# Optimization experiments

Hardware: AMD Instinct MI355X
Metric: run time of the kernel (lower is better)

## Reference

```python
import jax, jax.numpy as jnp
import numpy as np


def setup_inputs() -> dict:
    key = jax.random.key(0)
    k1, k2 = jax.random.split(key)
    N, C, K = 65536, 128, 1024  # N = batch*emb_sample_len flattened latents
    z_e = jax.random.normal(k1, (N, C), dtype=jnp.float32)
    # nn.Embedding codebook; original inits uniform(-1/K, 1/K), randn is fine for a numeric reference
    codebook = jax.random.normal(k2, (K, C), dtype=jnp.float32) * 0.02
    return {"z_e": z_e, "codebook": codebook}


def reference(z_e, codebook):
    """VQ-VAE quantizer core: cdist + argmin nearest-codebook lookup,
    commitment loss (0.75 * q_latent + e_latent), straight-through estimator.
    z_e: [N, C] flattened encoder latents; codebook: [K, C].
    """
    # Squared euclidean distances, expanded form (same argmin as torch.cdist)
    ze_sq = jnp.sum(z_e * z_e, axis=1, keepdims=True)          # [N, 1]
    cb_sq = jnp.sum(codebook * codebook, axis=1)                # [K]
    cross = jnp.einsum('nc,kc->nk', z_e, codebook)              # [N, K]
    dist_sq = ze_sq - 2.0 * cross + cb_sq[None, :]              # [N, K]
    encoding_indices = jnp.argmin(dist_sq, axis=1)              # [N] int

    z_q = codebook[encoding_indices]                            # [N, C] gather

    # commitment loss: 0.75 * mse(stop_grad(z_e), z_q) + mse(z_e, stop_grad(z_q))
    q_latent_loss = jnp.mean((jax.lax.stop_gradient(z_e) - z_q) ** 2)
    e_latent_loss = jnp.mean((z_e - jax.lax.stop_gradient(z_q)) ** 2)
    commitment_loss = 0.75 * q_latent_loss + e_latent_loss

    # straight-through estimator (training path)
    z_q_st = z_e + jax.lax.stop_gradient(z_q - z_e)
    return z_q_st, commitment_loss, encoding_indices
```

## Files before the change

### kernel.cpp

```cpp
#include <hip/hip_runtime.h>

#define N_TOT 65536
#define C_DIM 128
#define K_CB  1024
#define BN 64
#define BT 64
#define NTILE (K_CB / BT)
#define NROW_B 4
#define NBLK_B (N_TOT / NROW_B)

typedef __attribute__((ext_vector_type(8))) short bf16x8;
typedef __attribute__((ext_vector_type(4))) float f32x4;

__device__ __forceinline__ ushort f2bf_rne(float f) {
  unsigned u = __float_as_uint(f);
  return (ushort)((u + 0x7FFFu + ((u >> 16) & 1u)) >> 16);
}

__device__ __forceinline__ unsigned med3u(unsigned a, unsigned b, unsigned c) {
  unsigned d;
  asm("v_med3_u32 %0, %1, %2, %3" : "=v"(d) : "v"(a), "v"(b), "v"(c));
  return d;
}

#define GLDS16(src, dst)                                                       \
  __builtin_amdgcn_global_load_lds(                                            \
      (const __attribute__((address_space(1))) void*)(src),                    \
      (__attribute__((address_space(3))) void*)(dst), 16, 0, 0)

__global__ __launch_bounds__(256) void prep_kernel(
    const float* __restrict__ cb, float* __restrict__ cbsq,
    ushort* __restrict__ cbh) {
  int w = threadIdx.x >> 6, lane = threadIdx.x & 63;
  int r = blockIdx.x * 4 + w;
  float2 v = reinterpret_cast<const float2*>(cb + (size_t)r * C_DIM)[lane];
  ushort2 h;
  h.x = f2bf_rne(v.x); h.y = f2bf_rne(v.y);
  reinterpret_cast<ushort2*>(cbh + (size_t)r * C_DIM)[lane] = h;
  double s = (double)v.x * (double)v.x + (double)v.y * (double)v.y;
#pragma unroll
  for (int off = 32; off >= 1; off >>= 1) s += __shfl_xor(s, off, 64);
  if (lane == 0) cbsq[r] = (float)s;
}

__global__ __launch_bounds__(256, 4) void dist_mfma_kernel(
    const float* __restrict__ ze, const ushort* __restrict__ cbh,
    const float* __restrict__ cbsq, ushort* __restrict__ cand) {
  __shared__ __align__(16) char smem[36864];
  char* const B0 = smem;
  char* const B1 = smem + 16384;
  ushort* zhS = reinterpret_cast<ushort*>(B1);
  unsigned* pool = reinterpret_cast<unsigned*>(smem);
  float* const cbsqS = reinterpret_cast<float*>(smem + 32768);

  const int tid = threadIdx.x;
  const int w = tid >> 6, lane = tid & 63;
  const int mh = w & 1, nh = w >> 1;
  const int c16 = lane & 15, quad = lane >> 4;
  const int rowbase = blockIdx.x * BN;

  int soff[4];
#pragma unroll
  for (int i = 0; i < 4; ++i) {
    int o = w * 4096 + i * 1024 + lane * 16;
    int row = o >> 8, inrow = o & 255;
    soff[i] = row * 256 + (inrow ^ ((row & 7) << 4));
  }
  const int stoff = w * 4096;

#pragma unroll
  for (int i = 0; i < 4; ++i)
    GLDS16((const char*)cbh + soff[i], B0 + stoff + i * 1024);

#pragma unroll
  for (int p = 0; p < 4; ++p) {
    int fid = p * 256 + tid;
    int row = fid >> 4, c8 = fid & 15;
    float4 a = reinterpret_cast<const float4*>(ze)[(size_t)(rowbase + row) * 32 + c8 * 2];
    float4 b = reinterpret_cast<const float4*>(ze)[(size_t)(rowbase + row) * 32 + c8 * 2 + 1];
    ushort h[8] = {f2bf_rne(a.x), f2bf_rne(a.y), f2bf_rne(a.z), f2bf_rne(a.w),
                   f2bf_rne(b.x), f2bf_rne(b.y), f2bf_rne(b.z), f2bf_rne(b.w)};
    *reinterpret_cast<uint4*>(&zhS[row * 128 + ((c8 ^ (row & 7)) * 8)]) =
        *reinterpret_cast<const uint4*>(h);
  }
  reinterpret_cast<float4*>(cbsqS)[tid] = reinterpret_cast<const float4*>(cbsq)[tid];
  __syncthreads();

  const int xk = c16 & 7;
  bf16x8 afrag[2][4];
#pragma unroll
  for (int m2 = 0; m2 < 2; ++m2) {
    int r = (mh * 32 + m2 * 16 + c16) * 128;
#pragma unroll
    for (int ks = 0; ks < 4; ++ks)
      afrag[m2][ks] = *reinterpret_cast<const bf16x8*>(&zhS[r + ((ks * 4 + quad) ^ xk) * 8]);
  }
  __syncthreads();

  unsigned t3[8][3];
#pragma unroll
  for (int s = 0; s < 8; ++s) { t3[s][0] = 0xFFFFFFFFu; t3[s][1] = 0xFFFFFFFFu; t3[s][2] = 0xFFFFFFFFu; }

  const int cbase = nh * 32 + c16;
  const char* cur = B0;
  char* nxt = B1;

  for (int t = 0; t < NTILE; ++t) {
    if (t + 1 < NTILE) {
#pragma unroll
      for (int i = 0; i < 4; ++i)
        GLDS16((const char*)cbh + (size_t)(t + 1) * 16384 + soff[i], nxt + stoff + i * 1024);
    }

    bf16x8 bf[2][4];
#pragma unroll
    for (int n2 = 0; n2 < 2; ++n2) {
      int rb = (nh * 32 + n2 * 16 + c16) * 256;
#pragma unroll
      for (int ks = 0; ks < 4; ++ks)
        bf[n2][ks] = *reinterpret_cast<const bf16x8*>(cur + rb + (((ks * 4 + quad) ^ xk) << 4));
    }

    f32x4 acc[2][2];
#pragma unroll
    for (int m2 = 0; m2 < 2; ++m2)
#pragma unroll
      for (int n2 = 0; n2 < 2; ++n2) acc[m2][n2] = (f32x4){0.f, 0.f, 0.f, 0.f};

#pragma unroll
    for (int ks = 0; ks < 4; ++ks)
#pragma unroll
      for (int m2 = 0; m2 < 2; ++m2)
#pragma unroll
        for (int n2 = 0; n2 < 2; ++n2)
          acc[m2][n2] = __builtin_amdgcn_mfma_f32_16x16x32_bf16(afrag[m2][ks], bf[n2][ks], acc[m2][n2], 0, 0, 0);

#pragma unroll
    for (int n2 = 0; n2 < 2; ++n2) {
      int code = t * BT + cbase + n2 * 16;
      unsigned codeu = (unsigned)code & 1023u;
      float csb = cbsqS[code] + 192.0f;
#pragma unroll
      for (int m2 = 0; m2 < 2; ++m2)
#pragma unroll
        for (int reg = 0; reg < 4; ++reg) {
          float kf = fmaf(-2.f, acc[m2][n2][reg], csb);
          unsigned pk = (__float_as_uint(kf) & 0xFFFFFC00u) | codeu;
          int s = m2 * 4 + reg;
          unsigned n0 = min(t3[s][0], pk);
          unsigned n1 = med3u(t3[s][0], t3[s][1], pk);
          unsigned n2v = med3u(t3[s][1], t3[s][2], pk);
          t3[s][0] = n0; t3[s][1] = n1; t3[s][2] = n2v;
        }
    }

    __syncthreads();
    char* tmp = const_cast<char*>(cur); cur = nxt; nxt = tmp;
  }

#pragma unroll
  for (int s = 0; s < 8; ++s) {
    int row = mh * 32 + (s >> 2) * 16 + quad * 4 + (s & 3);
    int col = (nh * 16 + c16) * 3;
    pool[row * 97 + col] = t3[s][0];
    pool[row * 97 + col + 1] = t3[s][1];
    pool[row * 97 + col + 2] = t3[s][2];
  }
  __syncthreads();
  if (tid < BN) {
    unsigned k[8];
#pragma unroll
    for (int q = 0; q < 8; ++q) k[q] = 0xFFFFFFFFu;
    for (int p = 0; p < 96; ++p) {
      unsigned v = pool[tid * 97 + p];
      if (v < k[7]) {
        k[7] = v;
#pragma unroll
        for (int q = 7; q > 0; --q)
          if (k[q] < k[q - 1]) { unsigned tk = k[q]; k[q] = k[q - 1]; k[q - 1] = tk; }
      }
    }
    uint4 cw;
    cw.x = (k[0] & 1023u) | ((k[1] & 1023u) << 16);
    cw.y = (k[2] & 1023u) | ((k[3] & 1023u) << 16);
    cw.z = (k[4] & 1023u) | ((k[5] & 1023u) << 16);
    cw.w = (k[6] & 1023u) | ((k[7] & 1023u) << 16);
    reinterpret_cast<uint4*>(cand)[rowbase + tid] = cw;
  }
}

__global__ __launch_bounds__(256) void rescore_kernel(
    const float* __restrict__ ze, const float* __restrict__ cb,
    const float* __restrict__ cbsq, const ushort* __restrict__ cand,
    float* __restrict__ zq, float* __restrict__ idx_f,
    double* __restrict__ partial) {
  int w = threadIdx.x >> 6, lane = threadIdx.x & 63;
  int row = blockIdx.x * NROW_B + w;
  int g = lane >> 3, e = lane & 7;
  int myc = cand[(size_t)row * 8 + g];

  float2 z2 = reinterpret_cast<const float2*>(ze)[(size_t)row * 64 + lane];
  double zsum = (double)z2.x * (double)z2.x + (double)z2.y * (double)z2.y;
#pragma unroll
  for (int off = 32; off >= 1; off >>= 1) zsum += __shfl_xor(zsum, off, 64);
  float zs = (float)zsum;

  const float4* zrow4 = reinterpret_cast<const float4*>(ze + (size_t)row * C_DIM);
  const float4* crow4 = reinterpret_cast<const float4*>(cb + (size_t)myc * C_DIM);
  double p = 0.0;
#pragma unroll
  for (int q = 0; q < 4; ++q) {
    float4 zz = zrow4[e * 4 + q];
    float4 cc = crow4[e * 4 + q];
    p += (double)zz.x * (double)cc.x + (double)zz.y * (double)cc.y +
         (double)zz.z * (double)cc.z + (double)zz.w * (double)cc.w;
  }
  p += __shfl_xor(p, 1, 64);
  p += __shfl_xor(p, 2, 64);
  p += __shfl_xor(p, 4, 64);

  float tt = (float)(2.0 * p);
  float u = zs - tt;
  float d = u + cbsq[myc];

  float best = 3.4e38f;
  int bidx = K_CB + 1;
#pragma unroll
  for (int gg = 0; gg < 8; ++gg) {
    float dg = __shfl(d, gg * 8, 64);
    int ig = __shfl(myc, gg * 8, 64);
    if (dg < best || (dg == best && ig < bidx)) { best = dg; bidx = ig; }
  }

  float2 c2 = reinterpret_cast<const float2*>(cb)[(size_t)bidx * 64 + lane];
  reinterpret_cast<float2*>(zq)[(size_t)row * 64 + lane] = c2;

  double dx = (double)z2.x - (double)c2.x;
  double dy = (double)z2.y - (double)c2.y;
  double l = dx * dx + dy * dy;
#pragma unroll
  for (int off = 32; off >= 1; off >>= 1) l += __shfl_xor(l, off, 64);

  __shared__ double sh[NROW_B];
  if (lane == 0) { idx_f[row] = (float)bidx; sh[w] = l; }
  __syncthreads();
  if (threadIdx.x == 0) partial[blockIdx.x] = sh[0] + sh[1] + sh[2] + sh[3];
}

__global__ __launch_bounds__(256) void finalize_kernel(
    const double* __restrict__ partial, float* __restrict__ out_loss) {
  double s = 0.0;
  for (int i = threadIdx.x; i < NBLK_B; i += 256) s += partial[i];
#pragma unroll
  for (int off = 32; off >= 1; off >>= 1) s += __shfl_down(s, off, 64);
  __shared__ double sh[4];
  int wv = threadIdx.x >> 6, lane = threadIdx.x & 63;
  if (lane == 0) sh[wv] = s;
  __syncthreads();
  if (threadIdx.x == 0) {
    double tot = sh[0] + sh[1] + sh[2] + sh[3];
    double mse = tot / (double)((size_t)N_TOT * C_DIM);
    *out_loss = (float)(1.75 * mse);
  }
}

extern "C" void kernel_launch(void* const* d_in, const int* in_sizes, int n_in,
                              void* d_out, int out_size, void* d_ws, size_t ws_size,
                              hipStream_t stream) {
  const float* ze = (const float*)d_in[0];
  const float* cb = (const float*)d_in[1];

  float* out = (float*)d_out;
  float* zq = out;
  float* out_loss = out + (size_t)N_TOT * C_DIM;
  float* idx_f = out_loss + 1;

  float* cbsq = (float*)d_ws;
  ushort* cbh = (ushort*)((char*)d_ws + 8192);
  ushort* cand = (ushort*)((char*)d_ws + 270336);
  double* partial = (double*)((char*)d_ws + 1318912);

  prep_kernel<<<K_CB / 4, 256, 0, stream>>>(cb, cbsq, cbh);
  dist_mfma_kernel<<<N_TOT / BN, 256, 0, stream>>>(ze, cbh, cbsq, cand);
  rescore_kernel<<<NBLK_B, 256, 0, stream>>>(ze, cb, cbsq, cand, zq, idx_f, partial);
  finalize_kernel<<<1, 256, 0, stream>>>(partial, out_loss);
}
```

Before: 165.7 us.

## Software-pipeline distance MFMA with top-k sort and batch two rows per rescore wave

The distance kernel's tile loop is restructured into a two-accumulator software pipeline. The top-3 selection for tile t-1 now runs while the MFMAs for tile t are issued, and the loop is unrolled in pairs over the double buffers. The rescore kernel now has each wave handle two rows, with interleaved reductions and split dot-product accumulators to raise ILP. This halves the rescore block count and the number of partials. In exchange it uses more registers, which may lower occupancy.

Result: faster. 159.2 us (-3.9%).

```diff
diff --git a/kernel.cpp b/kernel.cpp
--- a/kernel.cpp
+++ b/kernel.cpp
@@ -6,8 +6,8 @@
 #define BN 64
 #define BT 64
 #define NTILE (K_CB / BT)
-#define NROW_B 4
-#define NBLK_B (N_TOT / NROW_B)
+#define ROWS_BLK 8
+#define NBLK_R (N_TOT / ROWS_BLK)
 
 typedef __attribute__((ext_vector_type(8))) short bf16x8;
 typedef __attribute__((ext_vector_type(4))) float f32x4;
@@ -102,31 +102,25 @@
   for (int s = 0; s < 8; ++s) { t3[s][0] = 0xFFFFFFFFu; t3[s][1] = 0xFFFFFFFFu; t3[s][2] = 0xFFFFFFFFu; }
 
   const int cbase = nh * 32 + c16;
-  const char* cur = B0;
-  char* nxt = B1;
-
-  for (int t = 0; t < NTILE; ++t) {
-    if (t + 1 < NTILE) {
-#pragma unroll
-      for (int i = 0; i < 4; ++i)
-        GLDS16((const char*)cbh + (size_t)(t + 1) * 16384 + soff[i], nxt + stoff + i * 1024);
-    }
-
+
+  auto STAGE = [&](int t, char* dst) {
+#pragma unroll
+    for (int i = 0; i < 4; ++i)
+      GLDS16((const char*)cbh + (size_t)t * 16384 + soff[i], dst + stoff + i * 1024);
+  };
+  auto READ_MFMA = [&](const char* buf, f32x4 (&acc)[2][2]) {
     bf16x8 bf[2][4];
 #pragma unroll
     for (int n2 = 0; n2 < 2; ++n2) {
       int rb = (nh * 32 + n2 * 16 + c16) * 256;
 #pragma unroll
       for (int ks = 0; ks < 4; ++ks)
-        bf[n2][ks] = *reinterpret_cast<const bf16x8*>(cur + rb + (((ks * 4 + quad) ^ xk) << 4));
-    }
-
-    f32x4 acc[2][2];
+        bf[n2][ks] = *reinterpret_cast<const bf16x8*>(buf + rb + (((ks * 4 + quad) ^ xk) << 4));
+    }
 #pragma unroll
     for (int m2 = 0; m2 < 2; ++m2)
 #pragma unroll
       for (int n2 = 0; n2 < 2; ++n2) acc[m2][n2] = (f32x4){0.f, 0.f, 0.f, 0.f};
-
 #pragma unroll
     for (int ks = 0; ks < 4; ++ks)
 #pragma unroll
@@ -134,7 +128,8 @@
 #pragma unroll
         for (int n2 = 0; n2 < 2; ++n2)
           acc[m2][n2] = __builtin_amdgcn_mfma_f32_16x16x32_bf16(afrag[m2][ks], bf[n2][ks], acc[m2][n2], 0, 0, 0);
-
+  };
+  auto SORT = [&](const f32x4 (&acc)[2][2], int t) {
 #pragma unroll
     for (int n2 = 0; n2 < 2; ++n2) {
       int code = t * BT + cbase + n2 * 16;
@@ -153,10 +148,29 @@
           t3[s][0] = n0; t3[s][1] = n1; t3[s][2] = n2v;
         }
     }
-
+  };
+
+  f32x4 accA[2][2], accB[2][2];
+
+  STAGE(1, B1);
+  READ_MFMA(B0, accA);
+  __syncthreads();
+
+  for (int tp = 0; tp < 7; ++tp) {
+    int t = 2 * tp + 1;
+    STAGE(t + 1, B0);
+    SORT(accA, t - 1);
+    READ_MFMA(B1, accB);
     __syncthreads();
-    char* tmp = const_cast<char*>(cur); cur = nxt; nxt = tmp;
-  }
+    STAGE(t + 2, B1);
+    SORT(accB, t);
+    READ_MFMA(B0, accA);
+    __syncthreads();
+  }
+  SORT(accA, 14);
+  READ_MFMA(B1, accB);
+  SORT(accB, 15);
+  __syncthreads();
 
 #pragma unroll
   for (int s = 0; s < 8; ++s) {
@@ -195,62 +209,105 @@
     float* __restrict__ zq, float* __restrict__ idx_f,
     double* __restrict__ partial) {
   int w = threadIdx.x >> 6, lane = threadIdx.x & 63;
-  int row = blockIdx.x * NROW_B + w;
+  int rbase = blockIdx.x * ROWS_BLK + w * 2;
   int g = lane >> 3, e = lane & 7;
-  int myc = cand[(size_t)row * 8 + g];
-
-  float2 z2 = reinterpret_cast<const float2*>(ze)[(size_t)row * 64 + lane];
-  double zsum = (double)z2.x * (double)z2.x + (double)z2.y * (double)z2.y;
-#pragma unroll
-  for (int off = 32; off >= 1; off >>= 1) zsum += __shfl_xor(zsum, off, 64);
-  float zs = (float)zsum;
-
-  const float4* zrow4 = reinterpret_cast<const float4*>(ze + (size_t)row * C_DIM);
-  const float4* crow4 = reinterpret_cast<const float4*>(cb + (size_t)myc * C_DIM);
-  double p = 0.0;
-#pragma unroll
-  for (int q = 0; q < 4; ++q) {
-    float4 zz = zrow4[e * 4 + q];
-    float4 cc = crow4[e * 4 + q];
-    p += (double)zz.x * (double)cc.x + (double)zz.y * (double)cc.y +
-         (double)zz.z * (double)cc.z + (double)zz.w * (double)cc.w;
-  }
-  p += __shfl_xor(p, 1, 64);
-  p += __shfl_xor(p, 2, 64);
-  p += __shfl_xor(p, 4, 64);
-
-  float tt = (float)(2.0 * p);
-  float u = zs - tt;
-  float d = u + cbsq[myc];
-
-  float best = 3.4e38f;
-  int bidx = K_CB + 1;
+
+  int myc[2];
+  float2 z2[2];
+  double zsum[2];
+#pragma unroll
+  for (int r = 0; r < 2; ++r) {
+    myc[r] = cand[(size_t)(rbase + r) * 8 + g];
+    z2[r] = reinterpret_cast<const float2*>(ze)[(size_t)(rbase + r) * 64 + lane];
+    zsum[r] = (double)z2[r].x * (double)z2[r].x + (double)z2[r].y * (double)z2[r].y;
+  }
+#pragma unroll
+  for (int off = 32; off >= 1; off >>= 1) {
+    zsum[0] += __shfl_xor(zsum[0], off, 64);
+    zsum[1] += __shfl_xor(zsum[1], off, 64);
+  }
+
+  double p[2];
+#pragma unroll
+  for (int r = 0; r < 2; ++r) {
+    const float4* zr = reinterpret_cast<const float4*>(ze + (size_t)(rbase + r) * C_DIM);
+    const float4* cr = reinterpret_cast<const float4*>(cb + (size_t)myc[r] * C_DIM);
+    double p0 = 0.0, p1 = 0.0;
+#pragma unroll
+    for (int q = 0; q < 2; ++q) {
+      float4 zz = zr[e * 4 + q];
+      float4 cc = cr[e * 4 + q];
+      p0 += (double)zz.x * (double)cc.x + (double)zz.y * (double)cc.y +
+            (double)zz.z * (double)cc.z + (double)zz.w * (double)cc.w;
+      float4 zz2 = zr[e * 4 + 2 + q];
+      float4 cc2 = cr[e * 4 + 2 + q];
+      p1 += (double)zz2.x * (double)cc2.x + (double)zz2.y * (double)cc2.y +
+            (double)zz2.z * (double)cc2.z + (double)zz2.w * (double)cc2.w;
+    }
+    p[r] = p0 + p1;
+  }
+#pragma unroll
+  for (int off = 1; off <= 4; off <<= 1) {
+    p[0] += __shfl_xor(p[0], off, 64);
+    p[1] += __shfl_xor(p[1], off, 64);
+  }
+
+  float d[2];
+#pragma unroll
+  for (int r = 0; r < 2; ++r) {
+    float zs = (float)zsum[r];
+    float tt = (float)(2.0 * p[r]);
+    float u = zs - tt;
+    d[r] = u + cbsq[myc[r]];
+  }
+
+  float best[2];
+  int bidx[2];
+#pragma unroll
+  for (int r = 0; r < 2; ++r) { best[r] = 3.4e38f; bidx[r] = K_CB + 1; }
 #pragma unroll
   for (int gg = 0; gg < 8; ++gg) {
-    float dg = __shfl(d, gg * 8, 64);
-    int ig = __shfl(myc, gg * 8, 64);
-    if (dg < best || (dg == best && ig < bidx)) { best = dg; bidx = ig; }
-  }
-
-  float2 c2 = reinterpret_cast<const float2*>(cb)[(size_t)bidx * 64 + lane];
-  reinterpret_cast<float2*>(zq)[(size_t)row * 64 + lane] = c2;
-
-  double dx = (double)z2.x - (double)c2.x;
-  double dy = (double)z2.y - (double)c2.y;
-  double l = dx * dx + dy * dy;
-#pragma unroll
-  for (int off = 32; off >= 1; off >>= 1) l += __shfl_xor(l, off, 64);
-
-  __shared__ double sh[NROW_B];
-  if (lane == 0) { idx_f[row] = (float)bidx; sh[w] = l; }
-  __syncthreads();
-  if (threadIdx.x == 0) partial[blockIdx.x] = sh[0] + sh[1] + sh[2] + sh[3];
+#pragma unroll
+    for (int r = 0; r < 2; ++r) {
+      float dg = __shfl(d[r], gg * 8, 64);
+      int ig = __shfl(myc[r], gg * 8, 64);
+      if (dg < best[r] || (dg == best[r] && ig < bidx[r])) { best[r] = dg; bidx[r] = ig; }
+    }
+  }
+
+  double l[2];
+#pragma unroll
+  for (int r = 0; r < 2; ++r) {
+    float2 c2 = reinterpret_cast<const float2*>(cb)[(size_t)bidx[r] * 64 + lane];
+    reinterpret_cast<float2*>(zq)[(size_t)(rbase + r) * 64 + lane] = c2;
+    double dx = (double)z2[r].x - (double)c2.x;
+    double dy = (double)z2[r].y - (double)c2.y;
+    l[r] = dx * dx + dy * dy;
+  }
+#pragma unroll
+  for (int off = 32; off >= 1; off >>= 1) {
+    l[0] += __shfl_xor(l[0], off, 64);
+    l[1] += __shfl_xor(l[1], off, 64);
+  }
+
+  __shared__ double sh[ROWS_BLK];
+  if (lane == 0) {
+    idx_f[rbase] = (float)bidx[0];
+    idx_f[rbase + 1] = (float)bidx[1];
+    sh[w * 2] = l[0];
+    sh[w * 2 + 1] = l[1];
+  }
+  __syncthreads();
+  if (threadIdx.x == 0) {
+    partial[blockIdx.x] = ((sh[0] + sh[1]) + (sh[2] + sh[3])) +
+                          ((sh[4] + sh[5]) + (sh[6] + sh[7]));
+  }
 }
 
 __global__ __launch_bounds__(256) void finalize_kernel(
     const double* __restrict__ partial, float* __restrict__ out_loss) {
   double s = 0.0;
-  for (int i = threadIdx.x; i < NBLK_B; i += 256) s += partial[i];
+  for (int i = threadIdx.x; i < NBLK_R; i += 256) s += partial[i];
 #pragma unroll
   for (int off = 32; off >= 1; off >>= 1) s += __shfl_down(s, off, 64);
   __shared__ double sh[4];
@@ -282,6 +339,6 @@
 
   prep_kernel<<<K_CB / 4, 256, 0, stream>>>(cb, cbsq, cbh);
   dist_mfma_kernel<<<N_TOT / BN, 256, 0, stream>>>(ze, cbh, cbsq, cand);
-  rescore_kernel<<<NBLK_B, 256, 0, stream>>>(ze, cb, cbsq, cand, zq, idx_f, partial);
+  rescore_kernel<<<NBLK_R, 256, 0, stream>>>(ze, cb, cbsq, cand, zq, idx_f, partial);
   finalize_kernel<<<1, 256, 0, stream>>>(partial, out_loss);
 }
```

## Software-pipeline MFMA with top-3 sort and pack two rows per rescore wave

Applied to the files above, without the earlier changes.

The distance kernel's tile loop is restructured into a two-accumulator software pipeline. The top-3 selection for tile t-1 now runs while the MFMAs for tile t execute, so ALU sort work can overlap matrix-core work. The loop is unrolled in pairs over the double buffers. The rescore kernel now handles two rows per wavefront with float4 loads, computes the z norm inside the dot-product loop, and uses butterfly argmin shuffles, halving its block count. The cost is more accumulator registers in the distance kernel, which may lower occupancy.

After: 151.3 us. 1.1x faster.

```diff
diff --git a/kernel.cpp b/kernel.cpp
--- a/kernel.cpp
+++ b/kernel.cpp
@@ -6,8 +6,8 @@
 #define BN 64
 #define BT 64
 #define NTILE (K_CB / BT)
-#define NROW_B 4
-#define NBLK_B (N_TOT / NROW_B)
+#define ROWS_BLK 8
+#define NBLK_R (N_TOT / ROWS_BLK)
 
 typedef __attribute__((ext_vector_type(8))) short bf16x8;
 typedef __attribute__((ext_vector_type(4))) float f32x4;
@@ -102,31 +102,25 @@
   for (int s = 0; s < 8; ++s) { t3[s][0] = 0xFFFFFFFFu; t3[s][1] = 0xFFFFFFFFu; t3[s][2] = 0xFFFFFFFFu; }
 
   const int cbase = nh * 32 + c16;
-  const char* cur = B0;
-  char* nxt = B1;
-
-  for (int t = 0; t < NTILE; ++t) {
-    if (t + 1 < NTILE) {
-#pragma unroll
-      for (int i = 0; i < 4; ++i)
-        GLDS16((const char*)cbh + (size_t)(t + 1) * 16384 + soff[i], nxt + stoff + i * 1024);
-    }
-
+
+  auto STAGE = [&](int t, char* dst) {
+#pragma unroll
+    for (int i = 0; i < 4; ++i)
+      GLDS16((const char*)cbh + (size_t)t * 16384 + soff[i], dst + stoff + i * 1024);
+  };
+  auto READ_MFMA = [&](const char* buf, f32x4 (&acc)[2][2]) {
     bf16x8 bf[2][4];
 #pragma unroll
     for (int n2 = 0; n2 < 2; ++n2) {
       int rb = (nh * 32 + n2 * 16 + c16) * 256;
 #pragma unroll
       for (int ks = 0; ks < 4; ++ks)
-        bf[n2][ks] = *reinterpret_cast<const bf16x8*>(cur + rb + (((ks * 4 + quad) ^ xk) << 4));
+        bf[n2][ks] = *reinterpret_cast<const bf16x8*>(buf + rb + (((ks * 4 + quad) ^ xk) << 4));
     }
-
-    f32x4 acc[2][2];
 #pragma unroll
     for (int m2 = 0; m2 < 2; ++m2)
 #pragma unroll
       for (int n2 = 0; n2 < 2; ++n2) acc[m2][n2] = (f32x4){0.f, 0.f, 0.f, 0.f};
-
 #pragma unroll
     for (int ks = 0; ks < 4; ++ks)
 #pragma unroll
@@ -134,7 +128,8 @@
 #pragma unroll
         for (int n2 = 0; n2 < 2; ++n2)
           acc[m2][n2] = __builtin_amdgcn_mfma_f32_16x16x32_bf16(afrag[m2][ks], bf[n2][ks], acc[m2][n2], 0, 0, 0);
-
+  };
+  auto SORT = [&](const f32x4 (&acc)[2][2], int t) {
 #pragma unroll
     for (int n2 = 0; n2 < 2; ++n2) {
       int code = t * BT + cbase + n2 * 16;
@@ -153,10 +148,29 @@
           t3[s][0] = n0; t3[s][1] = n1; t3[s][2] = n2v;
         }
     }
-
+  };
+
+  f32x4 accA[2][2], accB[2][2];
+
+  STAGE(1, B1);
+  READ_MFMA(B0, accA);
+  __syncthreads();
+
+  for (int tp = 0; tp < 7; ++tp) {
+    int t = 2 * tp + 1;
+    STAGE(t + 1, B0);
+    SORT(accA, t - 1);
+    READ_MFMA(B1, accB);
     __syncthreads();
-    char* tmp = const_cast<char*>(cur); cur = nxt; nxt = tmp;
-  }
+    STAGE(t + 2, B1);
+    SORT(accB, t);
+    READ_MFMA(B0, accA);
+    __syncthreads();
+  }
+  SORT(accA, 14);
+  READ_MFMA(B1, accB);
+  SORT(accB, 15);
+  __syncthreads();
 
 #pragma unroll
   for (int s = 0; s < 8; ++s) {
@@ -195,62 +209,69 @@
     float* __restrict__ zq, float* __restrict__ idx_f,
     double* __restrict__ partial) {
   int w = threadIdx.x >> 6, lane = threadIdx.x & 63;
-  int row = blockIdx.x * NROW_B + w;
-  int g = lane >> 3, e = lane & 7;
+  int h = lane >> 5, sl = lane & 31;
+  int row = blockIdx.x * ROWS_BLK + w * 2 + h;
+  int g = sl >> 2, e = sl & 3;
   int myc = cand[(size_t)row * 8 + g];
 
-  float2 z2 = reinterpret_cast<const float2*>(ze)[(size_t)row * 64 + lane];
-  double zsum = (double)z2.x * (double)z2.x + (double)z2.y * (double)z2.y;
-#pragma unroll
-  for (int off = 32; off >= 1; off >>= 1) zsum += __shfl_xor(zsum, off, 64);
+  const float4* zr = reinterpret_cast<const float4*>(ze + (size_t)row * C_DIM);
+  const float4* cr = reinterpret_cast<const float4*>(cb + (size_t)myc * C_DIM);
+
+  double p0 = 0.0, p1 = 0.0, zs0 = 0.0, zs1 = 0.0;
+#pragma unroll
+  for (int j = 0; j < 8; ++j) {
+    float4 zf = zr[e + 4 * j];
+    float4 cf = cr[e + 4 * j];
+    double a = ((double)zf.x * (double)cf.x + (double)zf.y * (double)cf.y) +
+               ((double)zf.z * (double)cf.z + (double)zf.w * (double)cf.w);
+    double b = ((double)zf.x * (double)zf.x + (double)zf.y * (double)zf.y) +
+               ((double)zf.z * (double)zf.z + (double)zf.w * (double)zf.w);
+    if (j & 1) { p1 += a; zs1 += b; } else { p0 += a; zs0 += b; }
+  }
+  double pp = p0 + p1;
+  double zsum = zs0 + zs1;
+  pp += __shfl_xor(pp, 1, 64);
+  pp += __shfl_xor(pp, 2, 64);
+  zsum += __shfl_xor(zsum, 1, 64);
+  zsum += __shfl_xor(zsum, 2, 64);
+
   float zs = (float)zsum;
-
-  const float4* zrow4 = reinterpret_cast<const float4*>(ze + (size_t)row * C_DIM);
-  const float4* crow4 = reinterpret_cast<const float4*>(cb + (size_t)myc * C_DIM);
-  double p = 0.0;
-#pragma unroll
-  for (int q = 0; q < 4; ++q) {
-    float4 zz = zrow4[e * 4 + q];
-    float4 cc = crow4[e * 4 + q];
-    p += (double)zz.x * (double)cc.x + (double)zz.y * (double)cc.y +
-         (double)zz.z * (double)cc.z + (double)zz.w * (double)cc.w;
-  }
-  p += __shfl_xor(p, 1, 64);
-  p += __shfl_xor(p, 2, 64);
-  p += __shfl_xor(p, 4, 64);
-
-  float tt = (float)(2.0 * p);
+  float tt = (float)(2.0 * pp);
   float u = zs - tt;
   float d = u + cbsq[myc];
 
-  float best = 3.4e38f;
-  int bidx = K_CB + 1;
-#pragma unroll
-  for (int gg = 0; gg < 8; ++gg) {
-    float dg = __shfl(d, gg * 8, 64);
-    int ig = __shfl(myc, gg * 8, 64);
-    if (dg < best || (dg == best && ig < bidx)) { best = dg; bidx = ig; }
-  }
-
-  float2 c2 = reinterpret_cast<const float2*>(cb)[(size_t)bidx * 64 + lane];
-  reinterpret_cast<float2*>(zq)[(size_t)row * 64 + lane] = c2;
-
-  double dx = (double)z2.x - (double)c2.x;
-  double dy = (double)z2.y - (double)c2.y;
-  double l = dx * dx + dy * dy;
-#pragma unroll
-  for (int off = 32; off >= 1; off >>= 1) l += __shfl_xor(l, off, 64);
-
-  __shared__ double sh[NROW_B];
-  if (lane == 0) { idx_f[row] = (float)bidx; sh[w] = l; }
-  __syncthreads();
-  if (threadIdx.x == 0) partial[blockIdx.x] = sh[0] + sh[1] + sh[2] + sh[3];
+#pragma unroll
+  for (int off = 4; off <= 16; off <<= 1) {
+    float dg = __shfl_xor(d, off, 64);
+    int ig = __shfl_xor(myc, off, 64);
+    if (dg < d || (dg == d && ig < myc)) { d = dg; myc = ig; }
+  }
+
+  const float4* cbest = reinterpret_cast<const float4*>(cb + (size_t)myc * C_DIM);
+  float4 cl = cbest[sl];
+  float4 zl = zr[sl];
+  reinterpret_cast<float4*>(zq + (size_t)row * C_DIM)[sl] = cl;
+
+  double dx = (double)zl.x - (double)cl.x;
+  double dy = (double)zl.y - (double)cl.y;
+  double dz = (double)zl.z - (double)cl.z;
+  double dw = (double)zl.w - (double)cl.w;
+  double l = (dx * dx + dy * dy) + (dz * dz + dw * dw);
+#pragma unroll
+  for (int off = 1; off <= 32; off <<= 1) l += __shfl_xor(l, off, 64);
+
+  if (sl == 0) idx_f[row] = (float)myc;
+  __shared__ double sh[4];
+  if (lane == 0) sh[w] = l;
+  __syncthreads();
+  if (threadIdx.x == 0)
+    partial[blockIdx.x] = (sh[0] + sh[1]) + (sh[2] + sh[3]);
 }
 
 __global__ __launch_bounds__(256) void finalize_kernel(
     const double* __restrict__ partial, float* __restrict__ out_loss) {
   double s = 0.0;
-  for (int i = threadIdx.x; i < NBLK_B; i += 256) s += partial[i];
+  for (int i = threadIdx.x; i < NBLK_R; i += 256) s += partial[i];
 #pragma unroll
   for (int off = 32; off >= 1; off >>= 1) s += __shfl_down(s, off, 64);
   __shared__ double sh[4];
@@ -282,6 +303,6 @@
 
   prep_kernel<<<K_CB / 4, 256, 0, stream>>>(cb, cbsq, cbh);
   dist_mfma_kernel<<<N_TOT / BN, 256, 0, stream>>>(ze, cbh, cbsq, cand);
-  rescore_kernel<<<NBLK_B, 256, 0, stream>>>(ze, cb, cbsq, cand, zq, idx_f, partial);
+  rescore_kernel<<<NBLK_R, 256, 0, stream>>>(ze, cb, cbsq, cand, zq, idx_f, partial);
   finalize_kernel<<<1, 256, 0, stream>>>(partial, out_loss);
 }
```
